# Optimization experiments

Hardware: AMD Instinct MI355X
Metric: run time of the kernel (lower is better)

## Reference

```python
import jax, jax.numpy as jnp
import numpy as np

HEADS, DIM_KEY, DIM_VALUE, DIM, N, B = 8, 64, 192, 1536, 2048, 2
SCALE = DIM_KEY ** -0.5


def setup_inputs() -> dict:
    key = jax.random.key(0)
    ks = jax.random.split(key, 8)
    s = 0.02
    return {
        "x": jax.random.normal(ks[0], (B, N, DIM), jnp.float32),
        "Wq": jax.random.normal(ks[1], (DIM, HEADS * DIM_KEY), jnp.float32) * s,
        "Wk": jax.random.normal(ks[2], (DIM, HEADS * DIM_KEY), jnp.float32) * s,
        "Wv": jax.random.normal(ks[3], (DIM, HEADS * DIM_VALUE), jnp.float32) * s,
        "Wo": jax.random.normal(ks[4], (HEADS * DIM_VALUE, DIM), jnp.float32) * s,
        "bo": jnp.zeros((DIM,), jnp.float32),
        "pos_embed": jax.random.normal(ks[5], (HEADS, N, DIM_KEY), jnp.float32) * s,
        "rel_content_bias": jax.random.normal(ks[6], (1, HEADS, 1, DIM_KEY), jnp.float32),
    }


def _split_heads(t, d):
    # [B, N, H*d] -> [B, H, N, d]
    b, n, _ = t.shape
    return t.reshape(b, n, HEADS, d).transpose(0, 2, 1, 3)


def reference(x, Wq, Wk, Wv, Wo, bo, pos_embed, rel_content_bias):
    q = _split_heads(x @ Wq, DIM_KEY) * SCALE          # [B,H,N,dk]
    k = _split_heads(x @ Wk, DIM_KEY)                  # [B,H,N,dk]
    v = _split_heads(x @ Wv, DIM_VALUE)                # [B,H,N,dv]
    q_biased = q + pos_embed[None] + rel_content_bias  # additive biases fused into Q
    logits = jnp.einsum('bhid,bhjd->bhij', q_biased, k)
    attn = jax.nn.softmax(logits, axis=-1)
    out = jnp.einsum('bhij,bhjd->bhid', attn, v)       # [B,H,N,dv]
    out = out.transpose(0, 2, 1, 3).reshape(x.shape[0], x.shape[1], HEADS * DIM_VALUE)
    return out @ Wo + bo
```

## Files before the change

kernel.cpp:

```cpp
#include <hip/hip_runtime.h>

#define BB    2
#define HN    8
#define NSEQ  2048
#define DIMM  1536
#define DKD   64
#define DVD   192
#define QCOLS 512
#define VCOLS 1536

typedef short short8 __attribute__((ext_vector_type(8)));
typedef float f32x4  __attribute__((ext_vector_type(4)));
typedef unsigned short ushortT;

static __device__ inline ushortT f2bf(float f) {
    unsigned u = __builtin_bit_cast(unsigned, f);
    u = (u + 0x7FFFu + ((u >> 16) & 1u)) >> 16;
    return (ushortT)u;
}

static __device__ inline void gl_lds16(const ushortT* g, ushortT* l) {
    __builtin_amdgcn_global_load_lds(
        (const __attribute__((address_space(1))) unsigned int*)g,
        (__attribute__((address_space(3))) unsigned int*)l, 16, 0, 0);
}

__global__ __launch_bounds__(256)
void cvt_x_kernel(const float* __restrict__ x, ushortT* __restrict__ xb)
{
    const size_t idx = (size_t)blockIdx.x * 256 + threadIdx.x;
    const float4* p = (const float4*)x + idx * 2;
    const float4 a = p[0], b = p[1];
    short8 v;
    v[0] = f2bf(a.x); v[1] = f2bf(a.y); v[2] = f2bf(a.z); v[3] = f2bf(a.w);
    v[4] = f2bf(b.x); v[5] = f2bf(b.y); v[6] = f2bf(b.z); v[7] = f2bf(b.w);
    *(short8*)(xb + idx * 8) = v;
}

__global__ __launch_bounds__(256)
void trans_kernel(const float* __restrict__ W, ushortT* __restrict__ Wt, int ncols)
{
    __shared__ ushortT t[32][33];
    const int lx = threadIdx.x & 31, ly = threadIdx.x >> 5;
    const int c0 = blockIdx.x * 32, k0 = blockIdx.y * 32;
    #pragma unroll
    for (int r = 0; r < 4; r++) {
        const int k = k0 + ly + r * 8;
        t[ly + r * 8][lx] = f2bf(W[(size_t)k * ncols + c0 + lx]);
    }
    __syncthreads();
    #pragma unroll
    for (int r = 0; r < 4; r++) {
        const int c = c0 + ly + r * 8;
        Wt[(size_t)c * DIMM + k0 + lx] = t[lx][ly + r * 8];
    }
}

__global__ __launch_bounds__(256)
void gemm_kernel(const ushortT* __restrict__ A, const ushortT* __restrict__ Bt,
                 const float* __restrict__ bo,
                 const float* __restrict__ pos, const float* __restrict__ rcb,
                 ushortT* __restrict__ q_ws, ushortT* __restrict__ k_ws,
                 ushortT* __restrict__ v_ws, float* __restrict__ Cout, int mode)
{
    __shared__ ushortT As[128 * 32];
    __shared__ ushortT Bs[128 * 32];

    const int tid  = threadIdx.x;
    const int wave = tid >> 6, lane = tid & 63;
    const int quad = lane >> 4, l15 = lane & 15;
    const int wr = wave >> 1, wc = wave & 1;
    const int m0 = blockIdx.y * 128, n0 = blockIdx.x * 128;

    const int srow = lane >> 2;
    const int sch  = (lane & 3) * 8;

    f32x4 acc[4][4];
    #pragma unroll
    for (int i = 0; i < 4; i++)
        #pragma unroll
        for (int j = 0; j < 4; j++) acc[i][j] = (f32x4){0.f, 0.f, 0.f, 0.f};

    for (int k0 = 0; k0 < DIMM; k0 += 32) {
        #pragma unroll
        for (int t = 0; t < 2; t++) {
            const int s = wave * 2 + t;
            gl_lds16(A  + (size_t)(m0 + s * 16 + srow) * DIMM + k0 + sch, &As[s * 512]);
            gl_lds16(Bt + (size_t)(n0 + s * 16 + srow) * DIMM + k0 + sch, &Bs[s * 512]);
        }
        __syncthreads();

        short8 af[4], bf[4];
        #pragma unroll
        for (int i = 0; i < 4; i++)
            af[i] = *(const short8*)&As[(wr * 64 + i * 16 + l15) * 32 + quad * 8];
        #pragma unroll
        for (int j = 0; j < 4; j++)
            bf[j] = *(const short8*)&Bs[(wc * 64 + j * 16 + l15) * 32 + quad * 8];

        #pragma unroll
        for (int i = 0; i < 4; i++)
            #pragma unroll
            for (int j = 0; j < 4; j++)
                acc[i][j] = __builtin_amdgcn_mfma_f32_16x16x32_bf16(af[i], bf[j], acc[i][j], 0, 0, 0);

        __syncthreads();
    }

    #pragma unroll
    for (int i = 0; i < 4; i++) {
        #pragma unroll
        for (int j = 0; j < 4; j++) {
            const int gcol = n0 + wc * 64 + j * 16 + l15;
            #pragma unroll
            for (int r = 0; r < 4; r++) {
                const int grow = m0 + wr * 64 + i * 16 + quad * 4 + r;
                const float val = acc[i][j][r];
                if (mode == 1) {
                    Cout[(size_t)grow * DIMM + gcol] = val + bo[gcol];
                } else {
                    const int b = grow >> 11, n = grow & (NSEQ - 1);
                    if (gcol < QCOLS) {
                        const int h = gcol >> 6, d = gcol & 63;
                        q_ws[((size_t)(b * HN + h) * NSEQ + n) * DKD + d] =
                            f2bf(val * 0.125f + pos[((size_t)h * NSEQ + n) * DKD + d] + rcb[h * DKD + d]);
                    } else if (gcol < 2 * QCOLS) {
                        const int c = gcol - QCOLS, h = c >> 6, d = c & 63;
                        k_ws[((size_t)(b * HN + h) * NSEQ + n) * DKD + d] = f2bf(val);
                    } else {
                        const int c = gcol - 2 * QCOLS, h = c / DVD, d = c - h * DVD;
                        v_ws[((size_t)(b * HN + h) * DVD + d) * NSEQ + n] = f2bf(val);
                    }
                }
            }
        }
    }
}

#define KT 64
#define PLD 72
#define SHIFT 20.0f

__global__ __launch_bounds__(128)
void flash_kernel(const ushortT* __restrict__ q_ws, const ushortT* __restrict__ k_ws,
                  const ushortT* __restrict__ v_ws, ushortT* __restrict__ attn)
{
    __shared__ ushortT Ks[64 * 64];
    __shared__ ushortT Vs[192 * 64];
    __shared__ ushortT Ps[2 * 32 * PLD];

    const int tid = threadIdx.x;
    const int wave = tid >> 6, lane = tid & 63;
    const int quad = lane >> 4, l15 = lane & 15;

    const int bh = blockIdx.x >> 5;
    const int it = blockIdx.x & 31;
    const int n0 = it * 64;
    const int b  = bh >> 3, h = bh & 7;

    const ushortT* kg = k_ws + (size_t)bh * NSEQ * DKD;
    const ushortT* vg = v_ws + (size_t)bh * DVD * NSEQ;

    short8 qf[2][2];
    #pragma unroll
    for (int mt = 0; mt < 2; mt++)
        #pragma unroll
        for (int ks = 0; ks < 2; ks++) {
            const int row = n0 + wave * 32 + mt * 16 + l15;
            qf[mt][ks] = *(const short8*)(q_ws + ((size_t)bh * NSEQ + row) * DKD + ks * 32 + quad * 8);
        }

    f32x4 o[2][12];
    #pragma unroll
    for (int mt = 0; mt < 2; mt++)
        #pragma unroll
        for (int nt = 0; nt < 12; nt++) o[mt][nt] = (f32x4){0.f, 0.f, 0.f, 0.f};

    float l_part[2][4];
    #pragma unroll
    for (int mt = 0; mt < 2; mt++)
        #pragma unroll
        for (int i = 0; i < 4; i++) l_part[mt][i] = 0.f;

    ushortT* Pw = Ps + wave * (32 * PLD);

    const int sl_r  = lane >> 3;
    const int sl_ch = (lane & 7) ^ (sl_r & 7);

    for (int kt0 = 0; kt0 < NSEQ; kt0 += KT) {
        #pragma unroll
        for (int tt = 0; tt < 4; tt++) {
            const int t = wave * 4 + tt;
            gl_lds16(kg + ((size_t)(kt0 + t * 8 + sl_r)) * DKD + sl_ch * 8, &Ks[t * 512]);
        }
        #pragma unroll
        for (int uu = 0; uu < 12; uu++) {
            const int u = wave * 12 + uu;
            gl_lds16(vg + (size_t)(u * 8 + sl_r) * NSEQ + kt0 + sl_ch * 8, &Vs[u * 512]);
        }
        __syncthreads();

        f32x4 s[2][4];
        #pragma unroll
        for (int mt = 0; mt < 2; mt++)
            #pragma unroll
            for (int nt = 0; nt < 4; nt++) s[mt][nt] = (f32x4){0.f, 0.f, 0.f, 0.f};

        #pragma unroll
        for (int ks = 0; ks < 2; ks++) {
            #pragma unroll
            for (int nt = 0; nt < 4; nt++) {
                const int key = nt * 16 + l15;
                const int ch  = ks * 4 + quad;
                const int phys = key * 8 + (ch ^ (key & 7));
                short8 kf = *(const short8*)&Ks[phys * 8];
                s[0][nt] = __builtin_amdgcn_mfma_f32_16x16x32_bf16(qf[0][ks], kf, s[0][nt], 0, 0, 0);
                s[1][nt] = __builtin_amdgcn_mfma_f32_16x16x32_bf16(qf[1][ks], kf, s[1][nt], 0, 0, 0);
            }
        }

        #pragma unroll
        for (int mt = 0; mt < 2; mt++)
            #pragma unroll
            for (int nt = 0; nt < 4; nt++)
                #pragma unroll
                for (int i = 0; i < 4; i++) {
                    const float p = __expf(s[mt][nt][i] - SHIFT);
                    s[mt][nt][i] = p;
                    l_part[mt][i] += p;
                }

        #pragma unroll
        for (int mt = 0; mt < 2; mt++)
            #pragma unroll
            for (int nt = 0; nt < 4; nt++)
                #pragma unroll
                for (int i = 0; i < 4; i++)
                    Pw[(mt * 16 + quad * 4 + i) * PLD + nt * 16 + l15] = f2bf(s[mt][nt][i]);

        short8 a[2][2];
        #pragma unroll
        for (int mt = 0; mt < 2; mt++)
            #pragma unroll
            for (int ks2 = 0; ks2 < 2; ks2++)
                a[mt][ks2] = *(const short8*)&Pw[(mt * 16 + l15) * PLD + ks2 * 32 + quad * 8];

        #pragma unroll
        for (int nt2 = 0; nt2 < 12; nt2++) {
            #pragma unroll
            for (int ks2 = 0; ks2 < 2; ks2++) {
                const int d = nt2 * 16 + l15;
                const int ch = ks2 * 4 + quad;
                const int phys = d * 8 + (ch ^ (d & 7));
                short8 vf = *(const short8*)&Vs[phys * 8];
                o[0][nt2] = __builtin_amdgcn_mfma_f32_16x16x32_bf16(a[0][ks2], vf, o[0][nt2], 0, 0, 0);
                o[1][nt2] = __builtin_amdgcn_mfma_f32_16x16x32_bf16(a[1][ks2], vf, o[1][nt2], 0, 0, 0);
            }
        }
        __syncthreads();
    }

    #pragma unroll
    for (int off = 1; off <= 8; off <<= 1)
        #pragma unroll
        for (int mt = 0; mt < 2; mt++)
            #pragma unroll
            for (int i = 0; i < 4; i++)
                l_part[mt][i] += __shfl_xor(l_part[mt][i], off, 64);

    float inv[2][4];
    #pragma unroll
    for (int mt = 0; mt < 2; mt++)
        #pragma unroll
        for (int i = 0; i < 4; i++) inv[mt][i] = 1.f / l_part[mt][i];

    #pragma unroll
    for (int mt = 0; mt < 2; mt++)
        #pragma unroll
        for (int nt2 = 0; nt2 < 12; nt2++)
            #pragma unroll
            for (int i = 0; i < 4; i++) {
                const int n = n0 + wave * 32 + mt * 16 + quad * 4 + i;
                attn[((size_t)b * NSEQ + n) * DIMM + h * DVD + nt2 * 16 + l15] =
                    f2bf(o[mt][nt2][i] * inv[mt][i]);
            }
}

extern "C" void kernel_launch(void* const* d_in, const int* in_sizes, int n_in,
                              void* d_out, int out_size, void* d_ws, size_t ws_size,
                              hipStream_t stream)
{
    const float* x   = (const float*)d_in[0];
    const float* Wq  = (const float*)d_in[1];
    const float* Wk  = (const float*)d_in[2];
    const float* Wv  = (const float*)d_in[3];
    const float* Wo  = (const float*)d_in[4];
    const float* bo  = (const float*)d_in[5];
    const float* pos = (const float*)d_in[6];
    const float* rcb = (const float*)d_in[7];
    float* out = (float*)d_out;

    ushortT* xb    = (ushortT*)d_ws;
    ushortT* wqkv  = xb    + (size_t)4096 * DIMM;
    ushortT* wo_t  = wqkv  + (size_t)(2 * QCOLS + VCOLS) * DIMM;
    ushortT* q_ws  = wo_t  + (size_t)DIMM * DIMM;
    ushortT* k_ws  = q_ws  + (size_t)BB * HN * NSEQ * DKD;
    ushortT* v_ws  = k_ws  + (size_t)BB * HN * NSEQ * DKD;
    ushortT* attnb = v_ws  + (size_t)BB * HN * NSEQ * DVD;

    cvt_x_kernel<<<dim3(3072), dim3(256), 0, stream>>>(x, xb);
    trans_kernel<<<dim3(16, 48), dim3(256), 0, stream>>>(Wq, wqkv, QCOLS);
    trans_kernel<<<dim3(16, 48), dim3(256), 0, stream>>>(Wk, wqkv + (size_t)QCOLS * DIMM, QCOLS);
    trans_kernel<<<dim3(48, 48), dim3(256), 0, stream>>>(Wv, wqkv + (size_t)2 * QCOLS * DIMM, VCOLS);
    trans_kernel<<<dim3(48, 48), dim3(256), 0, stream>>>(Wo, wo_t, DIMM);

    gemm_kernel<<<dim3(20, 32), dim3(256), 0, stream>>>(xb, wqkv, bo, pos, rcb,
                                                        q_ws, k_ws, v_ws, nullptr, 0);
    flash_kernel<<<dim3(BB * HN * (NSEQ / 64)), dim3(128), 0, stream>>>(q_ws, k_ws, v_ws, attnb);
    gemm_kernel<<<dim3(12, 32), dim3(256), 0, stream>>>(attnb, wo_t, bo, pos, rcb,
                                                        q_ws, k_ws, v_ws, out, 1);
}
```

Baseline: 318.6 us.

## Merge prep kernels and retile GEMM to 128x64 with K=64 swizzled LDS

Folds the x conversion and the four weight transposes into one prep kernel launch, which cuts four launches. The GEMM tile goes from 128x128 with K-step 32 to 128x64 with K-step 64. Each wave now owns 32 rows across all 64 columns, and an XOR swizzle on the LDS layout is meant to avoid bank conflicts. This doubles the grid for better CU occupancy on the small GEMMs and halves the number of barrier iterations. The cost is less operand reuse per tile.

Measured after the change: 264.9 us. 16.8% less time.

```diff
diff --git a/kernel.cpp b/kernel.cpp
--- a/kernel.cpp
+++ b/kernel.cpp
@@ -26,34 +26,42 @@
 }
 
 __global__ __launch_bounds__(256)
-void cvt_x_kernel(const float* __restrict__ x, ushortT* __restrict__ xb)
+void prep_kernel(const float* __restrict__ x,
+                 const float* __restrict__ Wq, const float* __restrict__ Wk,
+                 const float* __restrict__ Wv, const float* __restrict__ Wo,
+                 ushortT* __restrict__ xb, ushortT* __restrict__ wqkv,
+                 ushortT* __restrict__ wo_t)
 {
-    const size_t idx = (size_t)blockIdx.x * 256 + threadIdx.x;
-    const float4* p = (const float4*)x + idx * 2;
-    const float4 a = p[0], b = p[1];
-    short8 v;
-    v[0] = f2bf(a.x); v[1] = f2bf(a.y); v[2] = f2bf(a.z); v[3] = f2bf(a.w);
-    v[4] = f2bf(b.x); v[5] = f2bf(b.y); v[6] = f2bf(b.z); v[7] = f2bf(b.w);
-    *(short8*)(xb + idx * 8) = v;
-}
-
-__global__ __launch_bounds__(256)
-void trans_kernel(const float* __restrict__ W, ushortT* __restrict__ Wt, int ncols)
-{
-    __shared__ ushortT t[32][33];
-    const int lx = threadIdx.x & 31, ly = threadIdx.x >> 5;
-    const int c0 = blockIdx.x * 32, k0 = blockIdx.y * 32;
-    #pragma unroll
-    for (int r = 0; r < 4; r++) {
-        const int k = k0 + ly + r * 8;
-        t[ly + r * 8][lx] = f2bf(W[(size_t)k * ncols + c0 + lx]);
+    __shared__ ushortT tt[32][33];
+    const int b = blockIdx.x, tid = threadIdx.x;
+
+    if (b < 3072) {
+        const size_t idx = (size_t)b * 256 + tid;
+        const float4* p = (const float4*)x + idx * 2;
+        const float4 a = p[0], c = p[1];
+        short8 v;
+        v[0] = f2bf(a.x); v[1] = f2bf(a.y); v[2] = f2bf(a.z); v[3] = f2bf(a.w);
+        v[4] = f2bf(c.x); v[5] = f2bf(c.y); v[6] = f2bf(c.z); v[7] = f2bf(c.w);
+        *(short8*)(xb + idx * 8) = v;
+        return;
     }
+
+    const float* W; ushortT* Wt; int ncols, t;
+    if (b < 3840)      { W = Wq; Wt = wqkv;                          ncols = QCOLS; t = b - 3072; }
+    else if (b < 4608) { W = Wk; Wt = wqkv + (size_t)QCOLS * DIMM;   ncols = QCOLS; t = b - 3840; }
+    else if (b < 6912) { W = Wv; Wt = wqkv + (size_t)2*QCOLS * DIMM; ncols = VCOLS; t = b - 4608; }
+    else               { W = Wo; Wt = wo_t;                          ncols = DIMM;  t = b - 6912; }
+
+    const int nbx = ncols >> 5;
+    const int c0 = (t % nbx) * 32, k0 = (t / nbx) * 32;
+    const int lx = tid & 31, ly = tid >> 5;
+    #pragma unroll
+    for (int r = 0; r < 4; r++)
+        tt[ly + r * 8][lx] = f2bf(W[(size_t)(k0 + ly + r * 8) * ncols + c0 + lx]);
     __syncthreads();
     #pragma unroll
-    for (int r = 0; r < 4; r++) {
-        const int c = c0 + ly + r * 8;
-        Wt[(size_t)c * DIMM + k0 + lx] = t[lx][ly + r * 8];
-    }
+    for (int r = 0; r < 4; r++)
+        Wt[(size_t)(c0 + ly + r * 8) * DIMM + k0 + lx] = tt[lx][ly + r * 8];
 }
 
 __global__ __launch_bounds__(256)
@@ -63,58 +71,74 @@
                  ushortT* __restrict__ q_ws, ushortT* __restrict__ k_ws,
                  ushortT* __restrict__ v_ws, float* __restrict__ Cout, int mode)
 {
-    __shared__ ushortT As[128 * 32];
-    __shared__ ushortT Bs[128 * 32];
+    __shared__ ushortT As[128 * 64];
+    __shared__ ushortT Bs[64 * 64];
 
     const int tid  = threadIdx.x;
     const int wave = tid >> 6, lane = tid & 63;
     const int quad = lane >> 4, l15 = lane & 15;
-    const int wr = wave >> 1, wc = wave & 1;
-    const int m0 = blockIdx.y * 128, n0 = blockIdx.x * 128;
-
-    const int srow = lane >> 2;
-    const int sch  = (lane & 3) * 8;
-
-    f32x4 acc[4][4];
-    #pragma unroll
-    for (int i = 0; i < 4; i++)
+    const int m0 = blockIdx.y * 128, n0 = blockIdx.x * 64;
+
+    const int sl_r = lane >> 3;
+    const int sl_c = ((lane & 7) ^ sl_r) * 8;
+
+    const ushortT* Ab = A  + (size_t)m0 * DIMM;
+    const ushortT* Bb = Bt + (size_t)n0 * DIMM;
+
+    f32x4 acc[2][4];
+    #pragma unroll
+    for (int i = 0; i < 2; i++)
         #pragma unroll
         for (int j = 0; j < 4; j++) acc[i][j] = (f32x4){0.f, 0.f, 0.f, 0.f};
 
-    for (int k0 = 0; k0 < DIMM; k0 += 32) {
+    for (int k0 = 0; k0 < DIMM; k0 += 64) {
+        #pragma unroll
+        for (int t = 0; t < 4; t++) {
+            const int g = wave * 4 + t;
+            gl_lds16(Ab + (size_t)(g * 8 + sl_r) * DIMM + k0 + sl_c, &As[g * 512]);
+        }
         #pragma unroll
         for (int t = 0; t < 2; t++) {
-            const int s = wave * 2 + t;
-            gl_lds16(A  + (size_t)(m0 + s * 16 + srow) * DIMM + k0 + sch, &As[s * 512]);
-            gl_lds16(Bt + (size_t)(n0 + s * 16 + srow) * DIMM + k0 + sch, &Bs[s * 512]);
+            const int g = wave * 2 + t;
+            gl_lds16(Bb + (size_t)(g * 8 + sl_r) * DIMM + k0 + sl_c, &Bs[g * 512]);
         }
         __syncthreads();
 
-        short8 af[4], bf[4];
-        #pragma unroll
-        for (int i = 0; i < 4; i++)
-            af[i] = *(const short8*)&As[(wr * 64 + i * 16 + l15) * 32 + quad * 8];
-        #pragma unroll
-        for (int j = 0; j < 4; j++)
-            bf[j] = *(const short8*)&Bs[(wc * 64 + j * 16 + l15) * 32 + quad * 8];
-
-        #pragma unroll
-        for (int i = 0; i < 4; i++)
-            #pragma unroll
-            for (int j = 0; j < 4; j++)
-                acc[i][j] = __builtin_amdgcn_mfma_f32_16x16x32_bf16(af[i], bf[j], acc[i][j], 0, 0, 0);
+        short8 af[2][2], bf[4][2];
+        #pragma unroll
+        for (int i = 0; i < 2; i++) {
+            const int r = wave * 32 + i * 16 + l15;
+            #pragma unroll
+            for (int ks = 0; ks < 2; ks++)
+                af[i][ks] = *(const short8*)&As[r * 64 + ((ks * 4 + quad) ^ (l15 & 7)) * 8];
+        }
+        #pragma unroll
+        for (int j = 0; j < 4; j++) {
+            const int r = j * 16 + l15;
+            #pragma unroll
+            for (int ks = 0; ks < 2; ks++)
+                bf[j][ks] = *(const short8*)&Bs[r * 64 + ((ks * 4 + quad) ^ (l15 & 7)) * 8];
+        }
+
+        #pragma unroll
+        for (int ks = 0; ks < 2; ks++)
+            #pragma unroll
+            for (int i = 0; i < 2; i++)
+                #pragma unroll
+                for (int j = 0; j < 4; j++)
+                    acc[i][j] = __builtin_amdgcn_mfma_f32_16x16x32_bf16(af[i][ks], bf[j][ks], acc[i][j], 0, 0, 0);
 
         __syncthreads();
     }
 
     #pragma unroll
-    for (int i = 0; i < 4; i++) {
+    for (int i = 0; i < 2; i++) {
         #pragma unroll
         for (int j = 0; j < 4; j++) {
-            const int gcol = n0 + wc * 64 + j * 16 + l15;
+            const int gcol = n0 + j * 16 + l15;
             #pragma unroll
             for (int r = 0; r < 4; r++) {
-                const int grow = m0 + wr * 64 + i * 16 + quad * 4 + r;
+                const int grow = m0 + wave * 32 + i * 16 + quad * 4 + r;
                 const float val = acc[i][j][r];
                 if (mode == 1) {
                     Cout[(size_t)grow * DIMM + gcol] = val + bo[gcol];
@@ -308,15 +332,11 @@
     ushortT* v_ws  = k_ws  + (size_t)BB * HN * NSEQ * DKD;
     ushortT* attnb = v_ws  + (size_t)BB * HN * NSEQ * DVD;
 
-    cvt_x_kernel<<<dim3(3072), dim3(256), 0, stream>>>(x, xb);
-    trans_kernel<<<dim3(16, 48), dim3(256), 0, stream>>>(Wq, wqkv, QCOLS);
-    trans_kernel<<<dim3(16, 48), dim3(256), 0, stream>>>(Wk, wqkv + (size_t)QCOLS * DIMM, QCOLS);
-    trans_kernel<<<dim3(48, 48), dim3(256), 0, stream>>>(Wv, wqkv + (size_t)2 * QCOLS * DIMM, VCOLS);
-    trans_kernel<<<dim3(48, 48), dim3(256), 0, stream>>>(Wo, wo_t, DIMM);
-
-    gemm_kernel<<<dim3(20, 32), dim3(256), 0, stream>>>(xb, wqkv, bo, pos, rcb,
+    prep_kernel<<<dim3(9216), dim3(256), 0, stream>>>(x, Wq, Wk, Wv, Wo, xb, wqkv, wo_t);
+
+    gemm_kernel<<<dim3(40, 32), dim3(256), 0, stream>>>(xb, wqkv, bo, pos, rcb,
                                                         q_ws, k_ws, v_ws, nullptr, 0);
     flash_kernel<<<dim3(BB * HN * (NSEQ / 64)), dim3(128), 0, stream>>>(q_ws, k_ws, v_ws, attnb);
-    gemm_kernel<<<dim3(12, 32), dim3(256), 0, stream>>>(attnb, wo_t, bo, pos, rcb,
+    gemm_kernel<<<dim3(24, 32), dim3(256), 0, stream>>>(attnb, wo_t, bo, pos, rcb,
                                                         q_ws, k_ws, v_ws, out, 1);
 }
```
